# Performance work log

Hardware: AMD Instinct MI355X
Metric: run time of the kernel (lower is better)

## Reference

```python
import jax, jax.numpy as jnp
import numpy as np

LOW_DIM = 1024
PARAM_DIMS = [(1024, 768), (768,), (768, 256), (256,)]
BLOCK_DIMS = [int(np.prod(d)) for d in PARAM_DIMS]
TOTAL_DIM = int(sum(BLOCK_DIMS))          # 984064
LL = 1 << int(np.ceil(np.log2(TOTAL_DIM)))  # 1048576 = 2^20
BATCH = 32


def fwht(x):
    """Unnormalized fast Walsh-Hadamard transform over the last axis.

    x: [B, L], L a power of two. Butterfly stage order does not change the
    result (H_L = H_2^{\\otimes n}), so this matches the torch chunk/cat loop.
    """
    B, L = x.shape
    h = L // 2
    while h >= 1:
        x = x.reshape(B, -1, 2, h)
        a, b = x[:, :, 0, :], x[:, :, 1, :]
        x = jnp.stack([a + b, a - b], axis=2)
        h //= 2
    return x.reshape(B, L)


def setup_inputs() -> dict:
    key = jax.random.key(0)
    kz, kb, kg = jax.random.split(key, 3)
    z = jax.random.normal(kz, (BATCH, LOW_DIM), dtype=jnp.float32)
    # BB: random signs in {-1, +1}, as in make_fastfood_vars
    BB = jnp.where(jax.random.uniform(kb, (LL,)) < 0.5, -1.0, 1.0).astype(jnp.float32)
    GG = jax.random.normal(kg, (LL,), dtype=jnp.float32)
    Pi = jnp.asarray(np.random.default_rng(0).permutation(LL), dtype=jnp.int32)
    divisor = jnp.sqrt(LL * jnp.sum(GG ** 2)).astype(jnp.float32)
    return {"z": z, "BB": BB, "GG": GG, "divisor": divisor, "Pi": Pi}


def reference(z, BB, GG, divisor, Pi):
    # pad z from low_dim to LL
    dd = jnp.pad(z, ((0, 0), (0, LL - z.shape[1])))      # [B, LL]
    m = fwht(dd * BB[None, :])                           # H (B x)
    m = m[:, Pi] * GG[None, :]                           # G Pi H B x
    m = fwht(m)                                          # H G Pi H B x
    scale = divisor * np.float32(np.sqrt(float(TOTAL_DIM) / LL))
    delta = m[:, :TOTAL_DIM] / scale                     # [B, total_dim]
    outs = []
    off = 0
    for bd, pd in zip(BLOCK_DIMS, PARAM_DIMS):
        outs.append(delta[:, off:off + bd].reshape(-1, *pd))
        off += bd
    return tuple(outs)
```

## Files before the change

kernel.cpp:

```cpp
#include <hip/hip_runtime.h>
#include <math.h>


#define TS 33
#define TOTAL_DIM 984064
#define OUT_B0 786432
#define OUT_B1 787200
#define OUT_B2 983808
#define OFF1 25165824L
#define OFF2 25190400L
#define OFF3 31481856L

__device__ __forceinline__ void fwht1024_cols(float* tile, int tid) {
    const int col = tid & 31;
    const int mbase = tid >> 5;
    #pragma unroll
    for (int h = 1; h < 1024; h *= 4) {
        __syncthreads();
        const int d = h * TS;
        #pragma unroll
        for (int s = 0; s < 8; ++s) {
            const int m = mbase + (s << 5);
            const int lo = m & (h - 1);
            const int i0 = ((m - lo) << 2) + lo;
            const int p0 = i0 * TS + col;
            float a = tile[p0];
            float b = tile[p0 + d];
            float c = tile[p0 + 2 * d];
            float e = tile[p0 + 3 * d];
            float apb = a + b, amb = a - b, cpe = c + e, cme = c - e;
            tile[p0]         = apb + cpe;
            tile[p0 + d]     = amb + cme;
            tile[p0 + 2 * d] = apb - cpe;
            tile[p0 + 3 * d] = amb - cme;
        }
    }
    __syncthreads();
}

__global__ __launch_bounds__(1024) void k_y(const float* __restrict__ z,
                                            const float* __restrict__ BBv,
                                            float* __restrict__ y_t) {
    __shared__ float tile[1024 * TS];
    const int tid = threadIdx.x;
    #pragma unroll 4
    for (int s = 0; s < 32; ++s) {
        tile[tid * TS + s] = z[s * 1024 + tid] * BBv[tid];
    }
    fwht1024_cols(tile, tid);
    const int b = tid & 31;
    #pragma unroll 4
    for (int s = 0; s < 32; ++s) {
        const int i = (tid >> 5) + (s << 5);
        y_t[i * 32 + b] = tile[i * TS + b];
    }
}

__global__ __launch_bounds__(1024) void k_pass1(const float* __restrict__ y_t,
                                                const float* __restrict__ GG,
                                                const int* __restrict__ Pi,
                                                float* __restrict__ U) {
    __shared__ float tile[1024 * TS];
    __shared__ int   p_s[1024];
    __shared__ float g_s[1024];
    const int tid = threadIdx.x;
    const int kh = blockIdx.x;
    const long base = (long)kh << 10;
    p_s[tid] = Pi[base + tid] & 1023;
    g_s[tid] = GG[base + tid];
    __syncthreads();

    const int b = tid & 31;
    const int klbase = tid >> 5;
    #pragma unroll 4
    for (int s = 0; s < 32; ++s) {
        const int kl = klbase + (s << 5);
        tile[kl * TS + b] = y_t[p_s[kl] * 32 + b] * g_s[kl];
    }
    fwht1024_cols(tile, tid);
    const int b2 = tid >> 5;
    const int jlb = tid & 31;
    const long wbase = ((long)b2 * 1024 + kh) * 1024;
    #pragma unroll 4
    for (int s = 0; s < 32; ++s) {
        const int jl = jlb + (s << 5);
        U[wbase + jl] = tile[jl * TS + b2];
    }
}

__global__ __launch_bounds__(1024) void k_pass2(const float* __restrict__ U,
                                                const float* __restrict__ divisor,
                                                float* __restrict__ out) {
    __shared__ float tile[1024 * TS];
    const int tid = threadIdx.x;
    const int jl0 = blockIdx.x << 5;
    const int b   = blockIdx.y;
    const int jl = tid & 31;
    const int khbase = tid >> 5;
    const float* Ub = U + ((long)b << 20);
    #pragma unroll 4
    for (int s = 0; s < 32; ++s) {
        const int kh = khbase + (s << 5);
        tile[kh * TS + jl] = Ub[((long)kh << 10) + jl0 + jl];
    }
    fwht1024_cols(tile, tid);
    const float inv = 1.0f / (divisor[0] * sqrtf((float)TOTAL_DIM / 1048576.0f));
    const int jhbase = tid >> 5;
    #pragma unroll 2
    for (int s = 0; s < 31; ++s) {
        const int jh = jhbase + (s << 5);
        if (jh > 960) continue;
        const int j = (jh << 10) + jl0 + jl;
        long oidx;
        if (j < OUT_B0)      oidx = (long)b * 786432 + j;
        else if (j < OUT_B1) oidx = OFF1 + (long)b * 768 + (j - OUT_B0);
        else if (j < OUT_B2) oidx = OFF2 + (long)b * 196608 + (j - OUT_B1);
        else                 oidx = OFF3 + (long)b * 256 + (j - OUT_B2);
        out[oidx] = tile[jh * TS + jl] * inv;
    }
}

extern "C" void kernel_launch(void* const* d_in, const int* in_sizes, int n_in,
                              void* d_out, int out_size, void* d_ws, size_t ws_size,
                              hipStream_t stream) {
    const float* z   = (const float*)d_in[0];
    const float* BBv = (const float*)d_in[1];
    const float* GG  = (const float*)d_in[2];
    const float* dv  = (const float*)d_in[3];
    const int*   Pi  = (const int*)d_in[4];
    float* out = (float*)d_out;

    float* y_t = (float*)d_ws;
    float* U   = (float*)((char*)d_ws + (size_t)131072);

    k_y<<<1, 1024, 0, stream>>>(z, BBv, y_t);
    k_pass1<<<1024, 1024, 0, stream>>>(y_t, GG, Pi, U);
    k_pass2<<<dim3(32, 32), 1024, 0, stream>>>(U, dv, out);
}
```

Baseline: 271.2 us.

## Do 1024-point FWHT in registers with wave DPP/swizzle shuffles, halve tile width

Each 1024-point Walsh-Hadamard transform now runs inside a single 64-lane wave. Every lane holds 16 values in registers, and the butterfly stages use DPP, ds_swizzle and shfl_xor cross-lane exchanges instead of repeated LDS read/write passes with block-wide barriers. Tiles shrink from 32 to 16 columns, so the grids double (k_y 2 blocks, pass1 2x1024 blocks, pass2 64x32 blocks) and LDS per block is halved, which allows more blocks per CU. This removes LDS traffic and the synchronisation inside the transform, at the cost of an LDS transpose before and after and higher register pressure.

```diff
diff --git a/kernel.cpp b/kernel.cpp
--- a/kernel.cpp
+++ b/kernel.cpp
@@ -2,7 +2,7 @@
 #include <math.h>
 
 
-#define TS 33
+#define TS 17
 #define TOTAL_DIM 984064
 #define OUT_B0 786432
 #define OUT_B1 787200
@@ -11,31 +11,46 @@
 #define OFF2 25190400L
 #define OFF3 31481856L
 
-__device__ __forceinline__ void fwht1024_cols(float* tile, int tid) {
-    const int col = tid & 31;
-    const int mbase = tid >> 5;
+template<int CTRL>
+__device__ __forceinline__ float pdpp(float x) {
+    return __int_as_float(__builtin_amdgcn_update_dpp(
+        0, __float_as_int(x), CTRL, 0xF, 0xF, true));
+}
+template<int OFS>
+__device__ __forceinline__ float pswz(float x) {
+    return __int_as_float(__builtin_amdgcn_ds_swizzle(__float_as_int(x), OFS));
+}
+
+__device__ __forceinline__ void fwht_wave(float v[16], int lane) {
+    const float s1  = (lane & 1)  ? -1.f : 1.f;
+    const float s2  = (lane & 2)  ? -1.f : 1.f;
+    const float s4  = (lane & 4)  ? -1.f : 1.f;
+    const float s8  = (lane & 8)  ? -1.f : 1.f;
+    const float s16 = (lane & 16) ? -1.f : 1.f;
+    const float s32 = (lane & 32) ? -1.f : 1.f;
     #pragma unroll
-    for (int h = 1; h < 1024; h *= 4) {
-        __syncthreads();
-        const int d = h * TS;
+    for (int r = 0; r < 16; ++r) { float p = pdpp<0xB1>(v[r]);   v[r] = fmaf(s1,  v[r], p); }
+    #pragma unroll
+    for (int r = 0; r < 16; ++r) { float p = pdpp<0x4E>(v[r]);   v[r] = fmaf(s2,  v[r], p); }
+    #pragma unroll
+    for (int r = 0; r < 16; ++r) { float p = pswz<0x101F>(v[r]); v[r] = fmaf(s4,  v[r], p); }
+    #pragma unroll
+    for (int r = 0; r < 16; ++r) { float p = pswz<0x201F>(v[r]); v[r] = fmaf(s8,  v[r], p); }
+    #pragma unroll
+    for (int r = 0; r < 16; ++r) { float p = pswz<0x401F>(v[r]); v[r] = fmaf(s16, v[r], p); }
+    #pragma unroll
+    for (int r = 0; r < 16; ++r) { float p = __shfl_xor(v[r], 32, 64); v[r] = fmaf(s32, v[r], p); }
+    #pragma unroll
+    for (int m = 1; m <= 8; m <<= 1) {
         #pragma unroll
-        for (int s = 0; s < 8; ++s) {
-            const int m = mbase + (s << 5);
-            const int lo = m & (h - 1);
-            const int i0 = ((m - lo) << 2) + lo;
-            const int p0 = i0 * TS + col;
-            float a = tile[p0];
-            float b = tile[p0 + d];
-            float c = tile[p0 + 2 * d];
-            float e = tile[p0 + 3 * d];
-            float apb = a + b, amb = a - b, cpe = c + e, cme = c - e;
-            tile[p0]         = apb + cpe;
-            tile[p0 + d]     = amb + cme;
-            tile[p0 + 2 * d] = apb - cpe;
-            tile[p0 + 3 * d] = amb - cme;
+        for (int r = 0; r < 16; ++r) {
+            if (!(r & m)) {
+                float a = v[r], b = v[r | m];
+                v[r] = a + b;
+                v[r | m] = a - b;
+            }
         }
     }
-    __syncthreads();
 }
 
 __global__ __launch_bounds__(1024) void k_y(const float* __restrict__ z,
@@ -43,80 +58,91 @@
                                             float* __restrict__ y_t) {
     __shared__ float tile[1024 * TS];
     const int tid = threadIdx.x;
+    const int lane = tid & 63, w = tid >> 6;
+    const int b = (blockIdx.x << 4) + w;
+    float v[16];
+    #pragma unroll
+    for (int r = 0; r < 16; ++r) {
+        const int i = r * 64 + lane;
+        v[r] = z[(b << 10) + i] * BBv[i];
+    }
+    fwht_wave(v, lane);
+    #pragma unroll
+    for (int r = 0; r < 16; ++r) tile[(r * 64 + lane) * TS + w] = v[r];
+    __syncthreads();
+    const int bcol = tid & 15, i0 = tid >> 4;
     #pragma unroll 4
-    for (int s = 0; s < 32; ++s) {
-        tile[tid * TS + s] = z[s * 1024 + tid] * BBv[tid];
-    }
-    fwht1024_cols(tile, tid);
-    const int b = tid & 31;
-    #pragma unroll 4
-    for (int s = 0; s < 32; ++s) {
-        const int i = (tid >> 5) + (s << 5);
-        y_t[i * 32 + b] = tile[i * TS + b];
+    for (int s = 0; s < 16; ++s) {
+        const int i = i0 + (s << 6);
+        y_t[(i << 5) + (blockIdx.x << 4) + bcol] = tile[i * TS + bcol];
     }
 }
 
-__global__ __launch_bounds__(1024) void k_pass1(const float* __restrict__ y_t,
-                                                const float* __restrict__ GG,
-                                                const int* __restrict__ Pi,
-                                                float* __restrict__ U) {
+__global__ __launch_bounds__(1024, 8) void k_pass1(const float* __restrict__ y_t,
+                                                   const float* __restrict__ GG,
+                                                   const int* __restrict__ Pi,
+                                                   float* __restrict__ U) {
     __shared__ float tile[1024 * TS];
+    __shared__ float g_s[1024];
     __shared__ int   p_s[1024];
-    __shared__ float g_s[1024];
     const int tid = threadIdx.x;
-    const int kh = blockIdx.x;
-    const long base = (long)kh << 10;
-    p_s[tid] = Pi[base + tid] & 1023;
-    g_s[tid] = GG[base + tid];
+    const int kh = blockIdx.x, bg = blockIdx.y;
+    p_s[tid] = Pi[(kh << 10) + tid] & 1023;
+    g_s[tid] = GG[(kh << 10) + tid];
     __syncthreads();
-
-    const int b = tid & 31;
-    const int klbase = tid >> 5;
+    const int b = tid & 15, kl0 = tid >> 4;
     #pragma unroll 4
-    for (int s = 0; s < 32; ++s) {
-        const int kl = klbase + (s << 5);
-        tile[kl * TS + b] = y_t[p_s[kl] * 32 + b] * g_s[kl];
+    for (int s = 0; s < 16; ++s) {
+        const int kl = kl0 + (s << 6);
+        tile[kl * TS + b] = y_t[(p_s[kl] << 5) + (bg << 4) + b] * g_s[kl];
     }
-    fwht1024_cols(tile, tid);
-    const int b2 = tid >> 5;
-    const int jlb = tid & 31;
-    const long wbase = ((long)b2 * 1024 + kh) * 1024;
-    #pragma unroll 4
-    for (int s = 0; s < 32; ++s) {
-        const int jl = jlb + (s << 5);
-        U[wbase + jl] = tile[jl * TS + b2];
-    }
+    __syncthreads();
+    const int lane = tid & 63, w = tid >> 6;
+    float v[16];
+    #pragma unroll
+    for (int r = 0; r < 16; ++r) v[r] = tile[(r * 64 + lane) * TS + w];
+    fwht_wave(v, lane);
+    const long ub = ((long)((bg << 4) + w) << 20) + ((long)kh << 10);
+    #pragma unroll
+    for (int r = 0; r < 16; ++r) U[ub + r * 64 + lane] = v[r];
 }
 
-__global__ __launch_bounds__(1024) void k_pass2(const float* __restrict__ U,
-                                                const float* __restrict__ divisor,
-                                                float* __restrict__ out) {
+__global__ __launch_bounds__(1024, 8) void k_pass2(const float* __restrict__ U,
+                                                   const float* __restrict__ divisor,
+                                                   float* __restrict__ out) {
     __shared__ float tile[1024 * TS];
     const int tid = threadIdx.x;
-    const int jl0 = blockIdx.x << 5;
-    const int b   = blockIdx.y;
-    const int jl = tid & 31;
-    const int khbase = tid >> 5;
-    const float* Ub = U + ((long)b << 20);
+    const int jl0 = blockIdx.x << 4;
+    const int bb  = blockIdx.y;
+    const float* Ub = U + ((long)bb << 20);
+    const int jl = tid & 15, k0 = tid >> 4;
     #pragma unroll 4
-    for (int s = 0; s < 32; ++s) {
-        const int kh = khbase + (s << 5);
+    for (int s = 0; s < 16; ++s) {
+        const int kh = k0 + (s << 6);
         tile[kh * TS + jl] = Ub[((long)kh << 10) + jl0 + jl];
     }
-    fwht1024_cols(tile, tid);
+    __syncthreads();
+    const int lane = tid & 63, w = tid >> 6;
+    float v[16];
+    #pragma unroll
+    for (int r = 0; r < 16; ++r) v[r] = tile[(r * 64 + lane) * TS + w];
+    fwht_wave(v, lane);
     const float inv = 1.0f / (divisor[0] * sqrtf((float)TOTAL_DIM / 1048576.0f));
-    const int jhbase = tid >> 5;
+    #pragma unroll
+    for (int r = 0; r < 16; ++r) tile[(r * 64 + lane) * TS + w] = v[r] * inv;
+    __syncthreads();
     #pragma unroll 2
-    for (int s = 0; s < 31; ++s) {
-        const int jh = jhbase + (s << 5);
-        if (jh > 960) continue;
-        const int j = (jh << 10) + jl0 + jl;
-        long oidx;
-        if (j < OUT_B0)      oidx = (long)b * 786432 + j;
-        else if (j < OUT_B1) oidx = OFF1 + (long)b * 768 + (j - OUT_B0);
-        else if (j < OUT_B2) oidx = OFF2 + (long)b * 196608 + (j - OUT_B1);
-        else                 oidx = OFF3 + (long)b * 256 + (j - OUT_B2);
-        out[oidx] = tile[jh * TS + jl] * inv;
+    for (int s = 0; s < 16; ++s) {
+        const int jh = k0 + (s << 6);
+        if (jh <= 960) {
+            const int j = (jh << 10) + jl0 + jl;
+            long oidx;
+            if (j < OUT_B0)      oidx = (long)bb * 786432 + j;
+            else if (j < OUT_B1) oidx = OFF1 + (long)bb * 768 + (j - OUT_B0);
+            else if (j < OUT_B2) oidx = OFF2 + (long)bb * 196608 + (j - OUT_B1);
+            else                 oidx = OFF3 + (long)bb * 256 + (j - OUT_B2);
+            out[oidx] = tile[jh * TS + jl];
+        }
     }
 }
 
@@ -133,7 +159,7 @@
     float* y_t = (float*)d_ws;
     float* U   = (float*)((char*)d_ws + (size_t)131072);
 
-    k_y<<<1, 1024, 0, stream>>>(z, BBv, y_t);
-    k_pass1<<<1024, 1024, 0, stream>>>(y_t, GG, Pi, U);
-    k_pass2<<<dim3(32, 32), 1024, 0, stream>>>(U, dv, out);
+    k_y<<<2, 1024, 0, stream>>>(z, BBv, y_t);
+    k_pass1<<<dim3(1024, 2), 1024, 0, stream>>>(y_t, GG, Pi, U);
+    k_pass2<<<dim3(64, 32), 1024, 0, stream>>>(U, dv, out);
 }
```

Measured after the change: 246.5 us. -9.1%, faster.
